# Performance work log

Measured on AMD Instinct MI355X. Metric: run time of the kernel, lower is better.

## Reference

```python
import jax, jax.numpy as jnp
import numpy as np

N = 4096      # nodes
F = 512       # input_dim
D = 512       # output_dim
H = 8         # n_heads
d = D // H    # per-head out_sz


def setup_inputs() -> dict:
    key = jax.random.key(0)
    ks = jax.random.split(key, 6)
    x = jax.random.normal(ks[0], (N, F), dtype=jnp.float32)
    adj = (jax.random.uniform(ks[1], (N, N)) < 0.01).astype(jnp.float32)
    adj = jnp.maximum(adj, jnp.eye(N, dtype=jnp.float32))
    # per-head params: weight transform W, attention vectors a1/a2 (conv1d k=1 -> dot) with biases
    W = jax.random.normal(ks[2], (H, F, d), dtype=jnp.float32) * 0.05
    a1 = jax.random.normal(ks[3], (H, d), dtype=jnp.float32) * 0.05
    a2 = jax.random.normal(ks[4], (H, d), dtype=jnp.float32) * 0.05
    b1 = jnp.zeros((H,), dtype=jnp.float32)
    b2 = jnp.zeros((H,), dtype=jnp.float32)
    return {"x": x, "adj": adj, "W": W, "a1": a1, "b1": b1, "a2": a2, "b2": b2}


def reference(x, adj, W, a1, b1, a2, b2):
    # per-node linear transform for all heads: [H, N, d]
    seq_fts = jnp.einsum('nf,hfd->hnd', x, W)
    # attention logits components (conv1d(out=1,k=1) == dot + bias): [H, N]
    f1 = jnp.einsum('hnd,hd->hn', seq_fts, a1) + b1[:, None]
    f2 = jnp.einsum('hnd,hd->hn', seq_fts, a2) + b2[:, None]
    # logits = adj * f1_i + adj * f2_j  (adj acts multiplicatively AND as sparsity mask)
    logits = adj[None, :, :] * f1[:, :, None] + adj[None, :, :] * f2[:, None, :]
    lrelu = jnp.maximum(0.2 * logits, logits)  # leaky_relu alpha=0.2
    # sparse softmax over adjacency nonzeros (tf.sparse_softmax over from_dense pattern)
    mask = adj != 0
    scores = jnp.where(mask[None, :, :], lrelu, -jnp.inf)
    coefs = jax.nn.softmax(scores, axis=-1)           # [H, N, N], zero off-mask
    vals = jnp.einsum('hnm,hmd->hnd', coefs, seq_fts)  # sparse-dense matmul per head
    # concat heads on feature axis, batch dim of 1, elu activation
    h = jnp.transpose(vals, (1, 0, 2)).reshape(N, H * d)[None, :, :]
    return jax.nn.elu(h)
```

## Files before the change

kernel.cpp:

```cpp
#include <hip/hip_runtime.h>
#include <math.h>

#define N_NODES 4096
#define F_DIM   512
#define D_DIM   512
#define H_HEADS 8
#define HD      64
#define CAP     160

typedef __attribute__((ext_vector_type(8))) short short8;
typedef __attribute__((ext_vector_type(4))) float f32x4;

__device__ __forceinline__ unsigned short f2bf(float f) {
    unsigned int u = __builtin_bit_cast(unsigned int, f);
    return (unsigned short)((u + 0x7FFFu + ((u >> 16) & 1u)) >> 16);
}
__device__ __forceinline__ float bflo(unsigned int u) {
    return __builtin_bit_cast(float, u << 16);
}
__device__ __forceinline__ float bfhi(unsigned int u) {
    return __builtin_bit_cast(float, u & 0xffff0000u);
}

__global__ __launch_bounds__(256) void conv_inputs(const float* __restrict__ x,
                                                   const float* __restrict__ W,
                                                   unsigned short* __restrict__ xb,
                                                   unsigned short* __restrict__ Bt) {
    if (blockIdx.x < 1024) {
        const int t = blockIdx.x * 256 + threadIdx.x;
        const float4 v0 = *(const float4*)&x[t * 8];
        const float4 v1 = *(const float4*)&x[t * 8 + 4];
        unsigned short o[8] = {f2bf(v0.x), f2bf(v0.y), f2bf(v0.z), f2bf(v0.w),
                               f2bf(v1.x), f2bf(v1.y), f2bf(v1.z), f2bf(v1.w)};
        *(uint4*)&xb[t * 8] = *(const uint4*)o;
    } else {
        const int t = (blockIdx.x - 1024) * 256 + threadIdx.x;
        const int n = t >> 6;
        const int kb = (t & 63) * 8;
        const int h = n >> 6, dd = n & 63;
        const float* src = W + (size_t)h * F_DIM * HD + dd;
        unsigned short o[8];
        #pragma unroll
        for (int q = 0; q < 8; ++q) o[q] = f2bf(src[(size_t)(kb + q) * HD]);
        *(uint4*)&Bt[(size_t)n * F_DIM + kb] = *(const uint4*)o;
    }
}

__global__ __launch_bounds__(256) void gemm_plus(const unsigned short* __restrict__ A,
                                                 const unsigned short* __restrict__ Bt,
                                                 const float* __restrict__ adj,
                                                 const float* __restrict__ a1,
                                                 const float* __restrict__ b1,
                                                 const float* __restrict__ a2,
                                                 const float* __restrict__ b2,
                                                 unsigned short* __restrict__ seqb,
                                                 float* __restrict__ f1t,
                                                 float* __restrict__ f2t,
                                                 unsigned short* __restrict__ rowIdx,
                                                 int* __restrict__ cntArr) {
    __shared__ unsigned short As[64][40];
    __shared__ unsigned short Bs[64][40];
    __shared__ float sF[2][64][2];

    const int tid  = threadIdx.x;
    const int lane = tid & 63;
    const int w    = tid >> 6;

    if (blockIdx.x >= 512) {
        const int r = (blockIdx.x - 512) * 4 + w;
        const float* arow = adj + (size_t)r * N_NODES;

        f32x4 vq[16];
        #pragma unroll
        for (int q = 0; q < 16; ++q)
            vq[q] = *(const f32x4*)&arow[q * 256 + lane * 4];

        unsigned long long mask = 0ull;
        #pragma unroll
        for (int q = 0; q < 16; ++q) {
            if (vq[q].x != 0.0f) mask |= 1ull << (q * 4 + 0);
            if (vq[q].y != 0.0f) mask |= 1ull << (q * 4 + 1);
            if (vq[q].z != 0.0f) mask |= 1ull << (q * 4 + 2);
            if (vq[q].w != 0.0f) mask |= 1ull << (q * 4 + 3);
        }
        const int n_t = __popcll(mask);
        int incl = n_t;
        #pragma unroll
        for (int off = 1; off < 64; off <<= 1) {
            int u = __shfl_up(incl, off, 64);
            if (lane >= off) incl += u;
        }
        const int tot = __shfl(incl, 63, 64);
        int pos = incl - n_t;
        unsigned short* rbase = rowIdx + (size_t)r * CAP;
        while (mask) {
            const int bit = __builtin_ctzll(mask);
            mask &= mask - 1;
            const int col = ((bit >> 2) << 8) + (lane << 2) + (bit & 3);
            if (pos < CAP)
                __builtin_nontemporal_store((unsigned short)col, rbase + pos);
            ++pos;
        }
        if (lane == 0) cntArr[r] = tot;
        return;
    }

    const int wr   = w >> 1, wc = w & 1;
    const int i0   = (blockIdx.x & 63) * 64;
    const int h    = blockIdx.x >> 6;
    const int n0   = h * 64;

    const int ar = tid >> 2;
    const int ac = (tid & 3) * 8;

    const int rlane = lane & 15;
    const int q     = lane >> 4;
    const int klane = q * 8;

    f32x4 acc[2][2] = {};

    for (int k0 = 0; k0 < F_DIM; k0 += 32) {
        const uint4 av = *(const uint4*)&A[(size_t)(i0 + ar) * F_DIM + k0 + ac];
        const uint4 bv = *(const uint4*)&Bt[(size_t)(n0 + ar) * F_DIM + k0 + ac];
        __syncthreads();
        *(uint4*)&As[ar][ac] = av;
        *(uint4*)&Bs[ar][ac] = bv;
        __syncthreads();

        short8 a_frag[2], b_frag[2];
        #pragma unroll
        for (int mi = 0; mi < 2; ++mi)
            a_frag[mi] = *(const short8*)&As[wr * 32 + mi * 16 + rlane][klane];
        #pragma unroll
        for (int ni = 0; ni < 2; ++ni)
            b_frag[ni] = *(const short8*)&Bs[wc * 32 + ni * 16 + rlane][klane];
        #pragma unroll
        for (int mi = 0; mi < 2; ++mi)
            #pragma unroll
            for (int ni = 0; ni < 2; ++ni)
                acc[mi][ni] = __builtin_amdgcn_mfma_f32_16x16x32_bf16(
                    a_frag[mi], b_frag[ni], acc[mi][ni], 0, 0, 0);
    }

    #pragma unroll
    for (int mi = 0; mi < 2; ++mi)
        #pragma unroll
        for (int ni = 0; ni < 2; ++ni)
            #pragma unroll
            for (int r = 0; r < 4; ++r) {
                const int row = i0 + wr * 32 + mi * 16 + q * 4 + r;
                const int col = n0 + wc * 32 + ni * 16 + rlane;
                seqb[(size_t)row * D_DIM + col] = f2bf(acc[mi][ni][r]);
            }

    float a1v[2], a2v[2];
    #pragma unroll
    for (int ni = 0; ni < 2; ++ni) {
        const int c = wc * 32 + ni * 16 + rlane;
        a1v[ni] = a1[h * HD + c];
        a2v[ni] = a2[h * HD + c];
    }
    #pragma unroll
    for (int mi = 0; mi < 2; ++mi)
        #pragma unroll
        for (int r = 0; r < 4; ++r) {
            float s1 = acc[mi][0][r] * a1v[0] + acc[mi][1][r] * a1v[1];
            float s2 = acc[mi][0][r] * a2v[0] + acc[mi][1][r] * a2v[1];
            #pragma unroll
            for (int m = 1; m < 16; m <<= 1) {
                s1 += __shfl_xor(s1, m, 64);
                s2 += __shfl_xor(s2, m, 64);
            }
            if (rlane == 0) {
                const int rl = wr * 32 + mi * 16 + q * 4 + r;
                sF[0][rl][wc] = s1;
                sF[1][rl][wc] = s2;
            }
        }
    __syncthreads();
    if (tid < 64) {
        const int row = i0 + tid;
        f1t[row * 8 + h] = sF[0][tid][0] + sF[0][tid][1] + b1[h];
        f2t[row * 8 + h] = sF[1][tid][0] + sF[1][tid][1] + b2[h];
    }
}

__global__ __launch_bounds__(128) void attn(const float* __restrict__ adj,
                                            const unsigned short* __restrict__ seqb,
                                            const float* __restrict__ f1t,
                                            const float* __restrict__ f2t,
                                            const unsigned short* __restrict__ rowIdx,
                                            const int* __restrict__ cntArr,
                                            float* __restrict__ out) {
    __shared__ int   sIdx[CAP];
    __shared__ float sP[CAP][8];
    __shared__ float sRedM[2][8];
    __shared__ float sRedS[2][8];
    __shared__ float sAcc[64][8];

    const int i    = blockIdx.x;
    const int tid  = threadIdx.x;
    const int lane = tid & 63;
    const int w    = tid >> 6;

    const int cnt = cntArr[i];
    if (cnt <= CAP) {
        const unsigned short* rb = rowIdx + (size_t)i * CAP;
        for (int jj = tid; jj < cnt; jj += 128)
            sIdx[jj] = __builtin_nontemporal_load(rb + jj);
    }
    __syncthreads();

    const float4 f1a = *(const float4*)&f1t[i * 8];
    const float4 f1b = *(const float4*)&f1t[i * 8 + 4];
    const float f1r[8] = {f1a.x, f1a.y, f1a.z, f1a.w, f1b.x, f1b.y, f1b.z, f1b.w};

    const int h8 = lane >> 3;
    float acc[8] = {0.f, 0.f, 0.f, 0.f, 0.f, 0.f, 0.f, 0.f};
    float myinv;

    if (cnt <= CAP) {
        const bool has0 = tid < cnt;
        const bool has1 = tid + 128 < cnt;
        float L0[8], L1[8];
        float m[8];
        #pragma unroll
        for (int h = 0; h < 8; ++h) m[h] = -INFINITY;
        if (has0) {
            const int j = sIdx[tid];
            const float4 fa = *(const float4*)&f2t[j * 8];
            const float4 fb = *(const float4*)&f2t[j * 8 + 4];
            const float f2r[8] = {fa.x, fa.y, fa.z, fa.w, fb.x, fb.y, fb.z, fb.w};
            #pragma unroll
            for (int h = 0; h < 8; ++h) {
                float v = f1r[h] + f2r[h];
                v = fmaxf(v, 0.2f * v);
                L0[h] = v;
                m[h] = fmaxf(m[h], v);
            }
        }
        if (has1) {
            const int j = sIdx[tid + 128];
            const float4 fa = *(const float4*)&f2t[j * 8];
            const float4 fb = *(const float4*)&f2t[j * 8 + 4];
            const float f2r[8] = {fa.x, fa.y, fa.z, fa.w, fb.x, fb.y, fb.z, fb.w};
            #pragma unroll
            for (int h = 0; h < 8; ++h) {
                float v = f1r[h] + f2r[h];
                v = fmaxf(v, 0.2f * v);
                L1[h] = v;
                m[h] = fmaxf(m[h], v);
            }
        }
        #pragma unroll
        for (int off = 32; off; off >>= 1)
            #pragma unroll
            for (int h = 0; h < 8; ++h)
                m[h] = fmaxf(m[h], __shfl_xor(m[h], off, 64));
        if (lane == 0) {
            f32x4 ma = {m[0], m[1], m[2], m[3]};
            f32x4 mb = {m[4], m[5], m[6], m[7]};
            *(f32x4*)&sRedM[w][0] = ma;
            *(f32x4*)&sRedM[w][4] = mb;
        }
        __syncthreads();
        #pragma unroll
        for (int h = 0; h < 8; ++h) m[h] = fmaxf(sRedM[0][h], sRedM[1][h]);

        float s[8] = {0.f, 0.f, 0.f, 0.f, 0.f, 0.f, 0.f, 0.f};
        if (has0) {
            float e[8];
            #pragma unroll
            for (int h = 0; h < 8; ++h) {
                e[h] = __expf(L0[h] - m[h]);
                s[h] += e[h];
            }
            f32x4 ea = {e[0], e[1], e[2], e[3]};
            f32x4 eb = {e[4], e[5], e[6], e[7]};
            *(f32x4*)&sP[tid][0] = ea;
            *(f32x4*)&sP[tid][4] = eb;
        }
        if (has1) {
            float e[8];
            #pragma unroll
            for (int h = 0; h < 8; ++h) {
                e[h] = __expf(L1[h] - m[h]);
                s[h] += e[h];
            }
            f32x4 ea = {e[0], e[1], e[2], e[3]};
            f32x4 eb = {e[4], e[5], e[6], e[7]};
            *(f32x4*)&sP[tid + 128][0] = ea;
            *(f32x4*)&sP[tid + 128][4] = eb;
        }
        #pragma unroll
        for (int off = 32; off; off >>= 1)
            #pragma unroll
            for (int h = 0; h < 8; ++h)
                s[h] += __shfl_xor(s[h], off, 64);
        if (lane == 0) {
            f32x4 sa = {s[0], s[1], s[2], s[3]};
            f32x4 sb = {s[4], s[5], s[6], s[7]};
            *(f32x4*)&sRedS[w][0] = sa;
            *(f32x4*)&sRedS[w][4] = sb;
        }
        __syncthreads();
        myinv = 1.0f / (sRedS[0][h8] + sRedS[1][h8]);

        const int cnt2 = (cnt + 1) >> 1;
        const int jlo = w ? cnt2 : 0;
        const int jhi = w ? cnt  : cnt2;
        const char* __restrict__ vbase = (const char*)seqb + lane * 16;
        int jj = jlo;
        for (; jj + 8 <= jhi; jj += 8) {
            #pragma unroll
            for (int u2 = 0; u2 < 2; ++u2) {
                const int4 j4 = *(const int4*)&sIdx[jj + u2 * 4];
                const float p0 = sP[jj + u2 * 4 + 0][h8];
                const float p1 = sP[jj + u2 * 4 + 1][h8];
                const float p2 = sP[jj + u2 * 4 + 2][h8];
                const float p3 = sP[jj + u2 * 4 + 3][h8];
                const uint4 u0 = *(const uint4*)(vbase + ((size_t)j4.x << 10));
                const uint4 u1 = *(const uint4*)(vbase + ((size_t)j4.y << 10));
                const uint4 u2v = *(const uint4*)(vbase + ((size_t)j4.z << 10));
                const uint4 u3 = *(const uint4*)(vbase + ((size_t)j4.w << 10));
                const unsigned int w0[4] = {u0.x, u0.y, u0.z, u0.w};
                const unsigned int w1[4] = {u1.x, u1.y, u1.z, u1.w};
                const unsigned int w2[4] = {u2v.x, u2v.y, u2v.z, u2v.w};
                const unsigned int w3[4] = {u3.x, u3.y, u3.z, u3.w};
                #pragma unroll
                for (int k = 0; k < 4; ++k) {
                    acc[k * 2 + 0] = fmaf(p0, bflo(w0[k]), acc[k * 2 + 0]);
                    acc[k * 2 + 1] = fmaf(p0, bfhi(w0[k]), acc[k * 2 + 1]);
                    acc[k * 2 + 0] = fmaf(p1, bflo(w1[k]), acc[k * 2 + 0]);
                    acc[k * 2 + 1] = fmaf(p1, bfhi(w1[k]), acc[k * 2 + 1]);
                    acc[k * 2 + 0] = fmaf(p2, bflo(w2[k]), acc[k * 2 + 0]);
                    acc[k * 2 + 1] = fmaf(p2, bfhi(w2[k]), acc[k * 2 + 1]);
                    acc[k * 2 + 0] = fmaf(p3, bflo(w3[k]), acc[k * 2 + 0]);
                    acc[k * 2 + 1] = fmaf(p3, bfhi(w3[k]), acc[k * 2 + 1]);
                }
            }
        }
        for (; jj < jhi; ++jj) {
            const int j = sIdx[jj];
            const float p = sP[jj][h8];
            const uint4 u = *(const uint4*)(vbase + ((size_t)j << 10));
            const unsigned int wv[4] = {u.x, u.y, u.z, u.w};
            #pragma unroll
            for (int k = 0; k < 4; ++k) {
                acc[k * 2 + 0] = fmaf(p, bflo(wv[k]), acc[k * 2 + 0]);
                acc[k * 2 + 1] = fmaf(p, bfhi(wv[k]), acc[k * 2 + 1]);
            }
        }
    } else {
        const float* arow = adj + (size_t)i * N_NODES;
        float m[8];
        #pragma unroll
        for (int h = 0; h < 8; ++h) m[h] = -INFINITY;
        for (int j = tid; j < N_NODES; j += 128) {
            if (arow[j] != 0.0f) {
                const float4 fa = *(const float4*)&f2t[j * 8];
                const float4 fb = *(const float4*)&f2t[j * 8 + 4];
                const float f2r[8] = {fa.x, fa.y, fa.z, fa.w, fb.x, fb.y, fb.z, fb.w};
                #pragma unroll
                for (int h = 0; h < 8; ++h) {
                    float v = f1r[h] + f2r[h];
                    v = fmaxf(v, 0.2f * v);
                    m[h] = fmaxf(m[h], v);
                }
            }
        }
        #pragma unroll
        for (int off = 32; off; off >>= 1)
            #pragma unroll
            for (int h = 0; h < 8; ++h)
                m[h] = fmaxf(m[h], __shfl_xor(m[h], off, 64));
        if (lane == 0) {
            f32x4 ma = {m[0], m[1], m[2], m[3]};
            f32x4 mb = {m[4], m[5], m[6], m[7]};
            *(f32x4*)&sRedM[w][0] = ma;
            *(f32x4*)&sRedM[w][4] = mb;
        }
        __syncthreads();
        #pragma unroll
        for (int h = 0; h < 8; ++h) m[h] = fmaxf(sRedM[0][h], sRedM[1][h]);

        float s[8] = {0.f, 0.f, 0.f, 0.f, 0.f, 0.f, 0.f, 0.f};
        for (int j = tid; j < N_NODES; j += 128) {
            if (arow[j] != 0.0f) {
                const float4 fa = *(const float4*)&f2t[j * 8];
                const float4 fb = *(const float4*)&f2t[j * 8 + 4];
                const float f2r[8] = {fa.x, fa.y, fa.z, fa.w, fb.x, fb.y, fb.z, fb.w};
                #pragma unroll
                for (int h = 0; h < 8; ++h) {
                    float v = f1r[h] + f2r[h];
                    v = fmaxf(v, 0.2f * v);
                    s[h] += __expf(v - m[h]);
                }
            }
        }
        #pragma unroll
        for (int off = 32; off; off >>= 1)
            #pragma unroll
            for (int h = 0; h < 8; ++h)
                s[h] += __shfl_xor(s[h], off, 64);
        if (lane == 0) {
            f32x4 sa = {s[0], s[1], s[2], s[3]};
            f32x4 sb = {s[4], s[5], s[6], s[7]};
            *(f32x4*)&sRedS[w][0] = sa;
            *(f32x4*)&sRedS[w][4] = sb;
        }
        __syncthreads();
        myinv = 1.0f / (sRedS[0][h8] + sRedS[1][h8]);
        const float mh = m[h8], f1h = f1r[h8];

        const char* __restrict__ vbase = (const char*)seqb + lane * 16;
        const int jlo = w * (N_NODES / 2), jhi = jlo + N_NODES / 2;
        for (int j = jlo; j < jhi; ++j) {
            if (arow[j] != 0.0f) {
                float v = f1h + f2t[j * 8 + h8];
                v = fmaxf(v, 0.2f * v);
                const float p = __expf(v - mh);
                const uint4 u = *(const uint4*)(vbase + ((size_t)j << 10));
                const unsigned int wv[4] = {u.x, u.y, u.z, u.w};
                #pragma unroll
                for (int k = 0; k < 4; ++k) {
                    acc[k * 2 + 0] = fmaf(p, bflo(wv[k]), acc[k * 2 + 0]);
                    acc[k * 2 + 1] = fmaf(p, bfhi(wv[k]), acc[k * 2 + 1]);
                }
            }
        }
    }

    if (w == 1) {
        f32x4 pa = {acc[0], acc[1], acc[2], acc[3]};
        f32x4 pb = {acc[4], acc[5], acc[6], acc[7]};
        *(f32x4*)&sAcc[lane][0] = pa;
        *(f32x4*)&sAcc[lane][4] = pb;
    }
    __syncthreads();
    if (w == 0) {
        float o[8];
        #pragma unroll
        for (int k = 0; k < 8; ++k) {
            const float v = (acc[k] + sAcc[lane][k]) * myinv;
            o[k] = (v > 0.f) ? v : expm1f(v);
        }
        f32x4 oa = {o[0], o[1], o[2], o[3]};
        f32x4 ob = {o[4], o[5], o[6], o[7]};
        float* dst = &out[(size_t)i * D_DIM + lane * 8];
        __builtin_nontemporal_store(oa, (f32x4*)dst);
        __builtin_nontemporal_store(ob, (f32x4*)(dst + 4));
    }
}

extern "C" void kernel_launch(void* const* d_in, const int* in_sizes, int n_in,
                              void* d_out, int out_size, void* d_ws, size_t ws_size,
                              hipStream_t stream) {
    const float* x   = (const float*)d_in[0];
    const float* adj = (const float*)d_in[1];
    const float* W   = (const float*)d_in[2];
    const float* a1  = (const float*)d_in[3];
    const float* b1  = (const float*)d_in[4];
    const float* a2  = (const float*)d_in[5];
    const float* b2  = (const float*)d_in[6];
    float* out = (float*)d_out;

    char* ws = (char*)d_ws;
    unsigned short* seqb = (unsigned short*)ws;
    unsigned short* xb   = (unsigned short*)(ws + (size_t)N_NODES * D_DIM * 2);
    unsigned short* Bt   = (unsigned short*)(ws + (size_t)N_NODES * D_DIM * 4);
    float* f1t = (float*)(ws + (size_t)N_NODES * D_DIM * 4 + (size_t)D_DIM * F_DIM * 2);
    float* f2t = f1t + (size_t)N_NODES * H_HEADS;
    unsigned short* rowIdx = (unsigned short*)(f2t + (size_t)N_NODES * H_HEADS);
    int* cntArr = (int*)(rowIdx + (size_t)N_NODES * CAP);

    conv_inputs<<<1152, 256, 0, stream>>>(x, W, xb, Bt);

    gemm_plus<<<1536, 256, 0, stream>>>(xb, Bt, adj, a1, b1, a2, b2,
                                        seqb, f1t, f2t, rowIdx, cntArr);

    attn<<<N_NODES, 128, 0, stream>>>(adj, seqb, f1t, f2t, rowIdx, cntArr, out);
}
```

Baseline: 48.50 us.

## Fuse x bf16 conversion into GEMM, drop softmax max pass, pipeline gather

The x-to-bf16 conversion moves into the GEMM tile load, so the separate xb buffer and that part of the conversion kernel go away. The attention kernel stops subtracting the row max before exponentiation, which removes a reduction and a barrier, and it keeps each neighbour's weights in registers. The gather loop is restructured into groups of four with software prefetch of the next group. CAP shrinks to 128 so more rows take the slow dense fallback, and skipping the max subtraction risks overflow for large logits.

After: 43.95 us. 1.1x faster.

```diff
diff --git a/kernel.cpp b/kernel.cpp
--- a/kernel.cpp
+++ b/kernel.cpp
@@ -6,7 +6,7 @@
 #define D_DIM   512
 #define H_HEADS 8
 #define HD      64
-#define CAP     160
+#define CAP     128
 
 typedef __attribute__((ext_vector_type(8))) short short8;
 typedef __attribute__((ext_vector_type(4))) float f32x4;
@@ -22,42 +22,31 @@
     return __builtin_bit_cast(float, u & 0xffff0000u);
 }
 
-__global__ __launch_bounds__(256) void conv_inputs(const float* __restrict__ x,
-                                                   const float* __restrict__ W,
-                                                   unsigned short* __restrict__ xb,
-                                                   unsigned short* __restrict__ Bt) {
-    if (blockIdx.x < 1024) {
-        const int t = blockIdx.x * 256 + threadIdx.x;
-        const float4 v0 = *(const float4*)&x[t * 8];
-        const float4 v1 = *(const float4*)&x[t * 8 + 4];
-        unsigned short o[8] = {f2bf(v0.x), f2bf(v0.y), f2bf(v0.z), f2bf(v0.w),
-                               f2bf(v1.x), f2bf(v1.y), f2bf(v1.z), f2bf(v1.w)};
-        *(uint4*)&xb[t * 8] = *(const uint4*)o;
-    } else {
-        const int t = (blockIdx.x - 1024) * 256 + threadIdx.x;
-        const int n = t >> 6;
-        const int kb = (t & 63) * 8;
-        const int h = n >> 6, dd = n & 63;
-        const float* src = W + (size_t)h * F_DIM * HD + dd;
-        unsigned short o[8];
-        #pragma unroll
-        for (int q = 0; q < 8; ++q) o[q] = f2bf(src[(size_t)(kb + q) * HD]);
-        *(uint4*)&Bt[(size_t)n * F_DIM + kb] = *(const uint4*)o;
-    }
-}
-
-__global__ __launch_bounds__(256) void gemm_plus(const unsigned short* __restrict__ A,
-                                                 const unsigned short* __restrict__ Bt,
-                                                 const float* __restrict__ adj,
-                                                 const float* __restrict__ a1,
-                                                 const float* __restrict__ b1,
-                                                 const float* __restrict__ a2,
-                                                 const float* __restrict__ b2,
-                                                 unsigned short* __restrict__ seqb,
-                                                 float* __restrict__ f1t,
-                                                 float* __restrict__ f2t,
-                                                 unsigned short* __restrict__ rowIdx,
-                                                 int* __restrict__ cntArr) {
+__global__ __launch_bounds__(256) void conv_w(const float* __restrict__ W,
+                                              unsigned short* __restrict__ Bt) {
+    const int t = blockIdx.x * 256 + threadIdx.x;
+    const int n = t >> 6;
+    const int kb = (t & 63) * 8;
+    const int h = n >> 6, dd = n & 63;
+    const float* src = W + (size_t)h * F_DIM * HD + dd;
+    unsigned short o[8];
+    #pragma unroll
+    for (int q = 0; q < 8; ++q) o[q] = f2bf(src[(size_t)(kb + q) * HD]);
+    *(uint4*)&Bt[(size_t)n * F_DIM + kb] = *(const uint4*)o;
+}
+
+__global__ __launch_bounds__(256) void mega(const float* __restrict__ x,
+                                            const unsigned short* __restrict__ Bt,
+                                            const float* __restrict__ adj,
+                                            const float* __restrict__ a1,
+                                            const float* __restrict__ b1,
+                                            const float* __restrict__ a2,
+                                            const float* __restrict__ b2,
+                                            unsigned short* __restrict__ seqb,
+                                            float* __restrict__ f1t,
+                                            float* __restrict__ f2t,
+                                            unsigned short* __restrict__ rowIdx,
+                                            int* __restrict__ cntArr) {
     __shared__ unsigned short As[64][40];
     __shared__ unsigned short Bs[64][40];
     __shared__ float sF[2][64][2];
@@ -120,10 +109,14 @@
     f32x4 acc[2][2] = {};
 
     for (int k0 = 0; k0 < F_DIM; k0 += 32) {
-        const uint4 av = *(const uint4*)&A[(size_t)(i0 + ar) * F_DIM + k0 + ac];
+        const float* ga = &x[(size_t)(i0 + ar) * F_DIM + k0 + ac];
+        const float4 xa = *(const float4*)ga;
+        const float4 xb4 = *(const float4*)(ga + 4);
+        unsigned short ao[8] = {f2bf(xa.x), f2bf(xa.y), f2bf(xa.z), f2bf(xa.w),
+                                f2bf(xb4.x), f2bf(xb4.y), f2bf(xb4.z), f2bf(xb4.w)};
         const uint4 bv = *(const uint4*)&Bt[(size_t)(n0 + ar) * F_DIM + k0 + ac];
         __syncthreads();
-        *(uint4*)&As[ar][ac] = av;
+        *(uint4*)&As[ar][ac] = *(const uint4*)ao;
         *(uint4*)&Bs[ar][ac] = bv;
         __syncthreads();
 
@@ -194,7 +187,6 @@
                                             float* __restrict__ out) {
     __shared__ int   sIdx[CAP];
     __shared__ float sP[CAP][8];
-    __shared__ float sRedM[2][8];
     __shared__ float sRedS[2][8];
     __shared__ float sAcc[64][8];
 
@@ -202,32 +194,23 @@
     const int tid  = threadIdx.x;
     const int lane = tid & 63;
     const int w    = tid >> 6;
+    const int h8   = lane >> 3;
 
     const int cnt = cntArr[i];
-    if (cnt <= CAP) {
-        const unsigned short* rb = rowIdx + (size_t)i * CAP;
-        for (int jj = tid; jj < cnt; jj += 128)
-            sIdx[jj] = __builtin_nontemporal_load(rb + jj);
-    }
-    __syncthreads();
 
     const float4 f1a = *(const float4*)&f1t[i * 8];
     const float4 f1b = *(const float4*)&f1t[i * 8 + 4];
     const float f1r[8] = {f1a.x, f1a.y, f1a.z, f1a.w, f1b.x, f1b.y, f1b.z, f1b.w};
 
-    const int h8 = lane >> 3;
-    float acc[8] = {0.f, 0.f, 0.f, 0.f, 0.f, 0.f, 0.f, 0.f};
+    float accv[8] = {0.f, 0.f, 0.f, 0.f, 0.f, 0.f, 0.f, 0.f};
     float myinv;
 
     if (cnt <= CAP) {
-        const bool has0 = tid < cnt;
-        const bool has1 = tid + 128 < cnt;
-        float L0[8], L1[8];
-        float m[8];
-        #pragma unroll
-        for (int h = 0; h < 8; ++h) m[h] = -INFINITY;
-        if (has0) {
-            const int j = sIdx[tid];
+        int j = 0;
+        float s[8] = {0.f, 0.f, 0.f, 0.f, 0.f, 0.f, 0.f, 0.f};
+        float e[8] = {0.f, 0.f, 0.f, 0.f, 0.f, 0.f, 0.f, 0.f};
+        if (tid < cnt) {
+            j = (int)__builtin_nontemporal_load(rowIdx + (size_t)i * CAP + tid);
             const float4 fa = *(const float4*)&f2t[j * 8];
             const float4 fb = *(const float4*)&f2t[j * 8 + 4];
             const float f2r[8] = {fa.x, fa.y, fa.z, fa.w, fb.x, fb.y, fb.z, fb.w};
@@ -235,63 +218,16 @@
             for (int h = 0; h < 8; ++h) {
                 float v = f1r[h] + f2r[h];
                 v = fmaxf(v, 0.2f * v);
-                L0[h] = v;
-                m[h] = fmaxf(m[h], v);
-            }
-        }
-        if (has1) {
-            const int j = sIdx[tid + 128];
-            const float4 fa = *(const float4*)&f2t[j * 8];
-            const float4 fb = *(const float4*)&f2t[j * 8 + 4];
-            const float f2r[8] = {fa.x, fa.y, fa.z, fa.w, fb.x, fb.y, fb.z, fb.w};
-            #pragma unroll
-            for (int h = 0; h < 8; ++h) {
-                float v = f1r[h] + f2r[h];
-                v = fmaxf(v, 0.2f * v);
-                L1[h] = v;
-                m[h] = fmaxf(m[h], v);
-            }
-        }
-        #pragma unroll
-        for (int off = 32; off; off >>= 1)
-            #pragma unroll
-            for (int h = 0; h < 8; ++h)
-                m[h] = fmaxf(m[h], __shfl_xor(m[h], off, 64));
-        if (lane == 0) {
-            f32x4 ma = {m[0], m[1], m[2], m[3]};
-            f32x4 mb = {m[4], m[5], m[6], m[7]};
-            *(f32x4*)&sRedM[w][0] = ma;
-            *(f32x4*)&sRedM[w][4] = mb;
-        }
-        __syncthreads();
-        #pragma unroll
-        for (int h = 0; h < 8; ++h) m[h] = fmaxf(sRedM[0][h], sRedM[1][h]);
-
-        float s[8] = {0.f, 0.f, 0.f, 0.f, 0.f, 0.f, 0.f, 0.f};
-        if (has0) {
-            float e[8];
-            #pragma unroll
-            for (int h = 0; h < 8; ++h) {
-                e[h] = __expf(L0[h] - m[h]);
-                s[h] += e[h];
-            }
-            f32x4 ea = {e[0], e[1], e[2], e[3]};
-            f32x4 eb = {e[4], e[5], e[6], e[7]};
-            *(f32x4*)&sP[tid][0] = ea;
-            *(f32x4*)&sP[tid][4] = eb;
-        }
-        if (has1) {
-            float e[8];
-            #pragma unroll
-            for (int h = 0; h < 8; ++h) {
-                e[h] = __expf(L1[h] - m[h]);
-                s[h] += e[h];
-            }
-            f32x4 ea = {e[0], e[1], e[2], e[3]};
-            f32x4 eb = {e[4], e[5], e[6], e[7]};
-            *(f32x4*)&sP[tid + 128][0] = ea;
-            *(f32x4*)&sP[tid + 128][4] = eb;
-        }
+                e[h] = __expf(v);
+                s[h] = e[h];
+            }
+        }
+        sIdx[tid] = j;
+        f32x4 ea = {e[0], e[1], e[2], e[3]};
+        f32x4 eb = {e[4], e[5], e[6], e[7]};
+        *(f32x4*)&sP[tid][0] = ea;
+        *(f32x4*)&sP[tid][4] = eb;
+
         #pragma unroll
         for (int off = 32; off; off >>= 1)
             #pragma unroll
@@ -306,95 +242,70 @@
         __syncthreads();
         myinv = 1.0f / (sRedS[0][h8] + sRedS[1][h8]);
 
-        const int cnt2 = (cnt + 1) >> 1;
-        const int jlo = w ? cnt2 : 0;
-        const int jhi = w ? cnt  : cnt2;
+        const int G = (cnt + 3) >> 2;
         const char* __restrict__ vbase = (const char*)seqb + lane * 16;
-        int jj = jlo;
-        for (; jj + 8 <= jhi; jj += 8) {
-            #pragma unroll
-            for (int u2 = 0; u2 < 2; ++u2) {
-                const int4 j4 = *(const int4*)&sIdx[jj + u2 * 4];
-                const float p0 = sP[jj + u2 * 4 + 0][h8];
-                const float p1 = sP[jj + u2 * 4 + 1][h8];
-                const float p2 = sP[jj + u2 * 4 + 2][h8];
-                const float p3 = sP[jj + u2 * 4 + 3][h8];
-                const uint4 u0 = *(const uint4*)(vbase + ((size_t)j4.x << 10));
-                const uint4 u1 = *(const uint4*)(vbase + ((size_t)j4.y << 10));
-                const uint4 u2v = *(const uint4*)(vbase + ((size_t)j4.z << 10));
-                const uint4 u3 = *(const uint4*)(vbase + ((size_t)j4.w << 10));
+        int g = w;
+        if (g < G) {
+            int4 jC = *(const int4*)&sIdx[g * 4];
+            float pC0 = sP[g * 4 + 0][h8];
+            float pC1 = sP[g * 4 + 1][h8];
+            float pC2 = sP[g * 4 + 2][h8];
+            float pC3 = sP[g * 4 + 3][h8];
+            uint4 u0 = *(const uint4*)(vbase + ((size_t)jC.x << 10));
+            uint4 u1 = *(const uint4*)(vbase + ((size_t)jC.y << 10));
+            uint4 u2 = *(const uint4*)(vbase + ((size_t)jC.z << 10));
+            uint4 u3 = *(const uint4*)(vbase + ((size_t)jC.w << 10));
+            for (;;) {
+                const int gn = g + 2;
+                const bool more = gn < G;
+                int4 jN;
+                float pN0, pN1, pN2, pN3;
+                uint4 v0, v1, v2, v3;
+                if (more) {
+                    jN = *(const int4*)&sIdx[gn * 4];
+                    pN0 = sP[gn * 4 + 0][h8];
+                    pN1 = sP[gn * 4 + 1][h8];
+                    pN2 = sP[gn * 4 + 2][h8];
+                    pN3 = sP[gn * 4 + 3][h8];
+                    v0 = *(const uint4*)(vbase + ((size_t)jN.x << 10));
+                    v1 = *(const uint4*)(vbase + ((size_t)jN.y << 10));
+                    v2 = *(const uint4*)(vbase + ((size_t)jN.z << 10));
+                    v3 = *(const uint4*)(vbase + ((size_t)jN.w << 10));
+                }
                 const unsigned int w0[4] = {u0.x, u0.y, u0.z, u0.w};
                 const unsigned int w1[4] = {u1.x, u1.y, u1.z, u1.w};
-                const unsigned int w2[4] = {u2v.x, u2v.y, u2v.z, u2v.w};
+                const unsigned int w2[4] = {u2.x, u2.y, u2.z, u2.w};
                 const unsigned int w3[4] = {u3.x, u3.y, u3.z, u3.w};
                 #pragma unroll
                 for (int k = 0; k < 4; ++k) {
-                    acc[k * 2 + 0] = fmaf(p0, bflo(w0[k]), acc[k * 2 + 0]);
-                    acc[k * 2 + 1] = fmaf(p0, bfhi(w0[k]), acc[k * 2 + 1]);
-                    acc[k * 2 + 0] = fmaf(p1, bflo(w1[k]), acc[k * 2 + 0]);
-                    acc[k * 2 + 1] = fmaf(p1, bfhi(w1[k]), acc[k * 2 + 1]);
-                    acc[k * 2 + 0] = fmaf(p2, bflo(w2[k]), acc[k * 2 + 0]);
-                    acc[k * 2 + 1] = fmaf(p2, bfhi(w2[k]), acc[k * 2 + 1]);
-                    acc[k * 2 + 0] = fmaf(p3, bflo(w3[k]), acc[k * 2 + 0]);
-                    acc[k * 2 + 1] = fmaf(p3, bfhi(w3[k]), acc[k * 2 + 1]);
+                    accv[k * 2 + 0] = fmaf(pC0, bflo(w0[k]), accv[k * 2 + 0]);
+                    accv[k * 2 + 1] = fmaf(pC0, bfhi(w0[k]), accv[k * 2 + 1]);
+                    accv[k * 2 + 0] = fmaf(pC1, bflo(w1[k]), accv[k * 2 + 0]);
+                    accv[k * 2 + 1] = fmaf(pC1, bfhi(w1[k]), accv[k * 2 + 1]);
+                    accv[k * 2 + 0] = fmaf(pC2, bflo(w2[k]), accv[k * 2 + 0]);
+                    accv[k * 2 + 1] = fmaf(pC2, bfhi(w2[k]), accv[k * 2 + 1]);
+                    accv[k * 2 + 0] = fmaf(pC3, bflo(w3[k]), accv[k * 2 + 0]);
+                    accv[k * 2 + 1] = fmaf(pC3, bfhi(w3[k]), accv[k * 2 + 1]);
                 }
-            }
-        }
-        for (; jj < jhi; ++jj) {
-            const int j = sIdx[jj];
-            const float p = sP[jj][h8];
-            const uint4 u = *(const uint4*)(vbase + ((size_t)j << 10));
-            const unsigned int wv[4] = {u.x, u.y, u.z, u.w};
-            #pragma unroll
-            for (int k = 0; k < 4; ++k) {
-                acc[k * 2 + 0] = fmaf(p, bflo(wv[k]), acc[k * 2 + 0]);
-                acc[k * 2 + 1] = fmaf(p, bfhi(wv[k]), acc[k * 2 + 1]);
+                if (!more) break;
+                u0 = v0; u1 = v1; u2 = v2; u3 = v3;
+                pC0 = pN0; pC1 = pN1; pC2 = pN2; pC3 = pN3;
+                g = gn;
             }
         }
     } else {
         const float* arow = adj + (size_t)i * N_NODES;
-        float m[8];
-        #pragma unroll
-        for (int h = 0; h < 8; ++h) m[h] = -INFINITY;
-        for (int j = tid; j < N_NODES; j += 128) {
-            if (arow[j] != 0.0f) {
-                const float4 fa = *(const float4*)&f2t[j * 8];
-                const float4 fb = *(const float4*)&f2t[j * 8 + 4];
+        float s[8] = {0.f, 0.f, 0.f, 0.f, 0.f, 0.f, 0.f, 0.f};
+        for (int jx = tid; jx < N_NODES; jx += 128) {
+            if (arow[jx] != 0.0f) {
+                const float4 fa = *(const float4*)&f2t[jx * 8];
+                const float4 fb = *(const float4*)&f2t[jx * 8 + 4];
                 const float f2r[8] = {fa.x, fa.y, fa.z, fa.w, fb.x, fb.y, fb.z, fb.w};
                 #pragma unroll
                 for (int h = 0; h < 8; ++h) {
                     float v = f1r[h] + f2r[h];
                     v = fmaxf(v, 0.2f * v);
-                    m[h] = fmaxf(m[h], v);
-                }
-            }
-        }
-        #pragma unroll
-        for (int off = 32; off; off >>= 1)
-            #pragma unroll
-            for (int h = 0; h < 8; ++h)
-                m[h] = fmaxf(m[h], __shfl_xor(m[h], off, 64));
-        if (lane == 0) {
-            f32x4 ma = {m[0], m[1], m[2], m[3]};
-            f32x4 mb = {m[4], m[5], m[6], m[7]};
-            *(f32x4*)&sRedM[w][0] = ma;
-            *(f32x4*)&sRedM[w][4] = mb;
-        }
-        __syncthreads();
-        #pragma unroll
-        for (int h = 0; h < 8; ++h) m[h] = fmaxf(sRedM[0][h], sRedM[1][h]);
-
-        float s[8] = {0.f, 0.f, 0.f, 0.f, 0.f, 0.f, 0.f, 0.f};
-        for (int j = tid; j < N_NODES; j += 128) {
-            if (arow[j] != 0.0f) {
-                const float4 fa = *(const float4*)&f2t[j * 8];
-                const float4 fb = *(const float4*)&f2t[j * 8 + 4];
-                const float f2r[8] = {fa.x, fa.y, fa.z, fa.w, fb.x, fb.y, fb.z, fb.w};
-                #pragma unroll
-                for (int h = 0; h < 8; ++h) {
-                    float v = f1r[h] + f2r[h];
-                    v = fmaxf(v, 0.2f * v);
-                    s[h] += __expf(v - m[h]);
+                    s[h] += __expf(v);
                 }
             }
         }
@@ -411,29 +322,29 @@
         }
         __syncthreads();
         myinv = 1.0f / (sRedS[0][h8] + sRedS[1][h8]);
-        const float mh = m[h8], f1h = f1r[h8];
+        const float f1h = f1r[h8];
 
         const char* __restrict__ vbase = (const char*)seqb + lane * 16;
         const int jlo = w * (N_NODES / 2), jhi = jlo + N_NODES / 2;
-        for (int j = jlo; j < jhi; ++j) {
-            if (arow[j] != 0.0f) {
-                float v = f1h + f2t[j * 8 + h8];
+        for (int jx = jlo; jx < jhi; ++jx) {
+            if (arow[jx] != 0.0f) {
+                float v = f1h + f2t[jx * 8 + h8];
                 v = fmaxf(v, 0.2f * v);
-                const float p = __expf(v - mh);
-                const uint4 u = *(const uint4*)(vbase + ((size_t)j << 10));
+                const float p = __expf(v);
+                const uint4 u = *(const uint4*)(vbase + ((size_t)jx << 10));
                 const unsigned int wv[4] = {u.x, u.y, u.z, u.w};
                 #pragma unroll
                 for (int k = 0; k < 4; ++k) {
-                    acc[k * 2 + 0] = fmaf(p, bflo(wv[k]), acc[k * 2 + 0]);
-                    acc[k * 2 + 1] = fmaf(p, bfhi(wv[k]), acc[k * 2 + 1]);
+                    accv[k * 2 + 0] = fmaf(p, bflo(wv[k]), accv[k * 2 + 0]);
+                    accv[k * 2 + 1] = fmaf(p, bfhi(wv[k]), accv[k * 2 + 1]);
                 }
             }
         }
     }
 
     if (w == 1) {
-        f32x4 pa = {acc[0], acc[1], acc[2], acc[3]};
-        f32x4 pb = {acc[4], acc[5], acc[6], acc[7]};
+        f32x4 pa = {accv[0], accv[1], accv[2], accv[3]};
+        f32x4 pb = {accv[4], accv[5], accv[6], accv[7]};
         *(f32x4*)&sAcc[lane][0] = pa;
         *(f32x4*)&sAcc[lane][4] = pb;
     }
@@ -442,7 +353,7 @@
         float o[8];
         #pragma unroll
         for (int k = 0; k < 8; ++k) {
-            const float v = (acc[k] + sAcc[lane][k]) * myinv;
+            const float v = (accv[k] + sAcc[lane][k]) * myinv;
             o[k] = (v > 0.f) ? v : expm1f(v);
         }
         f32x4 oa = {o[0], o[1], o[2], o[3]};
@@ -467,17 +378,16 @@
 
     char* ws = (char*)d_ws;
     unsigned short* seqb = (unsigned short*)ws;
-    unsigned short* xb   = (unsigned short*)(ws + (size_t)N_NODES * D_DIM * 2);
-    unsigned short* Bt   = (unsigned short*)(ws + (size_t)N_NODES * D_DIM * 4);
-    float* f1t = (float*)(ws + (size_t)N_NODES * D_DIM * 4 + (size_t)D_DIM * F_DIM * 2);
+    unsigned short* Bt   = (unsigned short*)(ws + (size_t)N_NODES * D_DIM * 2);
+    float* f1t = (float*)(ws + (size_t)N_NODES * D_DIM * 2 + (size_t)D_DIM * F_DIM * 2);
     float* f2t = f1t + (size_t)N_NODES * H_HEADS;
     unsigned short* rowIdx = (unsigned short*)(f2t + (size_t)N_NODES * H_HEADS);
     int* cntArr = (int*)(rowIdx + (size_t)N_NODES * CAP);
 
-    conv_inputs<<<1152, 256, 0, stream>>>(x, W, xb, Bt);
-
-    gemm_plus<<<1536, 256, 0, stream>>>(xb, Bt, adj, a1, b1, a2, b2,
-                                        seqb, f1t, f2t, rowIdx, cntArr);
+    conv_w<<<128, 256, 0, stream>>>(W, Bt);
+
+    mega<<<1536, 256, 0, stream>>>(x, Bt, adj, a1, b1, a2, b2,
+                                   seqb, f1t, f2t, rowIdx, cntArr);
 
     attn<<<N_NODES, 128, 0, stream>>>(adj, seqb, f1t, f2t, rowIdx, cntArr, out);
 }
```
